# Optimization experiments

Measured on AMD Instinct MI355X. Metric: run time of the kernel, lower is better.

The kernel has to match this reference:

```python
import jax, jax.numpy as jnp
import numpy as np

DIM = 2048
STATE = 16
BATCH = 2
SEQ = 2048
LN_EPS = 1e-5


def setup_inputs() -> dict:
    key = jax.random.key(0)
    ks = jax.random.split(key, 12)
    d, n = DIM, STATE
    inp = {
        "x": jax.random.normal(ks[0], (BATCH, SEQ, d), dtype=jnp.float32),
        "ln_gamma": jnp.ones((d,), dtype=jnp.float32),
        "ln_beta": jnp.zeros((d,), dtype=jnp.float32),
        # proj_in: Linear(d, 2d) (spectral-normed; weights treated as effective)
        "W_in": jax.random.normal(ks[1], (2 * d, d), dtype=jnp.float32) / np.sqrt(d),
        "b_in": jnp.zeros((2 * d,), dtype=jnp.float32),
        "state_A": jax.random.normal(ks[2], (n, d), dtype=jnp.float32) * 0.01,
        "W_B": jax.random.normal(ks[3], (n, d), dtype=jnp.float32) / np.sqrt(d),
        "b_B": jnp.zeros((n,), dtype=jnp.float32),
        "W_C": jax.random.normal(ks[4], (n, d), dtype=jnp.float32) / np.sqrt(d),
        "b_C": jnp.zeros((n,), dtype=jnp.float32),
        "W_dt": jax.random.normal(ks[5], (d, d), dtype=jnp.float32) / np.sqrt(d),
        "b_dt": jnp.zeros((d,), dtype=jnp.float32),
        "W_out": jax.random.normal(ks[6], (d, d), dtype=jnp.float32) / np.sqrt(d),
        "b_out": jnp.zeros((d,), dtype=jnp.float32),
    }
    return inp


def reference(x, ln_gamma, ln_beta, W_in, b_in, state_A, W_B, b_B, W_C, b_C,
              W_dt, b_dt, W_out, b_out):
    residual = x
    # LayerNorm over last dim
    mu = jnp.mean(x, axis=-1, keepdims=True)
    var = jnp.mean(jnp.square(x - mu), axis=-1, keepdims=True)
    xn = (x - mu) * jax.lax.rsqrt(var + LN_EPS) * ln_gamma + ln_beta
    # input projection and gate split
    xz = jnp.einsum('bsd,ed->bse', xn, W_in) + b_in          # (B,S,2D)
    x_ssm, z = jnp.split(xz, 2, axis=-1)                      # (B,S,D) each
    # dt = clamp(softplus(proj_dt(x_ssm)), max=1.0)
    dt = jnp.minimum(jax.nn.softplus(jnp.einsum('bsd,ed->bse', x_ssm, W_dt) + b_dt), 1.0)
    Bm = jnp.einsum('bsd,nd->bsn', x_ssm, W_B) + b_B          # (B,S,N)
    Cm = jnp.einsum('bsd,nd->bsn', x_ssm, W_C) + b_C          # (B,S,N)
    # A_bar[b,s,n,d] = exp(state_A[n,d] * dt[b,s,d])
    A_bar = jnp.exp(state_A[None, None, :, :] * dt[:, :, None, :])  # (B,S,N,D)
    # y[b,s,d] = sum_n C[b,s,n]*B[b,s,n]*A_bar[b,s,n,d] * x_ssm[b,s,d]
    y = jnp.einsum('bsn,bsnd->bsd', Cm * Bm, A_bar) * x_ssm
    gated = y * jax.nn.silu(z)
    out = jnp.einsum('bsd,ed->bse', gated, W_out) + b_out
    return out + residual
```

## Files before the change

### kernel.cpp

```cpp
#include <hip/hip_runtime.h>

typedef unsigned short u16;
typedef float f32x4 __attribute__((ext_vector_type(4)));
typedef __bf16 bf16x8 __attribute__((ext_vector_type(8)));

__device__ __forceinline__ u16 f2bf(float f) {
    unsigned u = __float_as_uint(f);
    u += 0x7FFFu + ((u >> 16) & 1u);
    return (u16)(u >> 16);
}
__device__ __forceinline__ float b2f(u16 h) {
    return __uint_as_float(((unsigned)h) << 16);
}

__device__ __forceinline__ void async16(const u16* g, u16* l) {
    __builtin_amdgcn_global_load_lds(
        (__attribute__((address_space(1))) void*)(u16*)g,
        (__attribute__((address_space(3))) void*)l,
        16, 0, 0);
}

#define T_TOK 4096
#define DIM   2048

__global__ __launch_bounds__(256) void castln_kernel(const float* __restrict__ W_in,
                                                     u16* __restrict__ wb_in,
                                                     const float* __restrict__ x,
                                                     const float* __restrict__ g,
                                                     const float* __restrict__ b,
                                                     u16* __restrict__ o) {
    __shared__ float s1[4], s2[4];
    int blk = blockIdx.x, tid = threadIdx.x;
    if (blk < 8192) {
        int i = blk * 256 + tid;
        float4 f = ((const float4*)W_in)[i];
        ushort4 u;
        u.x = f2bf(f.x); u.y = f2bf(f.y); u.z = f2bf(f.z); u.w = f2bf(f.w);
        ((ushort4*)wb_in)[i] = u;
        return;
    }
    int t = blk - 8192;
    int wave = tid >> 6, lane = tid & 63;
    size_t base = (size_t)t * DIM;
    int d0 = tid * 8;
    float4 v0 = *(const float4*)(x + base + d0);
    float4 v1 = *(const float4*)(x + base + d0 + 4);
    float v[8] = {v0.x, v0.y, v0.z, v0.w, v1.x, v1.y, v1.z, v1.w};
    float s = 0.f;
#pragma unroll
    for (int j = 0; j < 8; ++j) s += v[j];
#pragma unroll
    for (int o2 = 32; o2; o2 >>= 1) s += __shfl_xor(s, o2);
    if (lane == 0) s1[wave] = s;
    __syncthreads();
    float mu = (s1[0] + s1[1] + s1[2] + s1[3]) * (1.f / DIM);
    float q = 0.f;
#pragma unroll
    for (int j = 0; j < 8; ++j) { float dd = v[j] - mu; q += dd * dd; }
#pragma unroll
    for (int o2 = 32; o2; o2 >>= 1) q += __shfl_xor(q, o2);
    if (lane == 0) s2[wave] = q;
    __syncthreads();
    float var = (s2[0] + s2[1] + s2[2] + s2[3]) * (1.f / DIM);
    float rs = rsqrtf(var + 1e-5f);
    float4 g0 = *(const float4*)(g + d0), g1 = *(const float4*)(g + d0 + 4);
    float4 b0 = *(const float4*)(b + d0), b1 = *(const float4*)(b + d0 + 4);
    float gv[8] = {g0.x, g0.y, g0.z, g0.w, g1.x, g1.y, g1.z, g1.w};
    float bv[8] = {b0.x, b0.y, b0.z, b0.w, b1.x, b1.y, b1.z, b1.w};
    ushort4 r0, r1;
    u16* rp0 = (u16*)&r0; u16* rp1 = (u16*)&r1;
#pragma unroll
    for (int j = 0; j < 4; ++j) {
        rp0[j] = f2bf((v[j] - mu) * rs * gv[j] + bv[j]);
        rp1[j] = f2bf((v[j + 4] - mu) * rs * gv[j + 4] + bv[j + 4]);
    }
    *(ushort4*)(o + base + d0) = r0;
    *(ushort4*)(o + base + d0 + 4) = r1;
}

__global__ __launch_bounds__(256) void cast4_kernel(const float* __restrict__ s0, u16* __restrict__ d0, int n0,
                                                    const float* __restrict__ s1, u16* __restrict__ d1, int n1,
                                                    const float* __restrict__ s2, u16* __restrict__ d2, int n2,
                                                    const float* __restrict__ s3, u16* __restrict__ d3, int n3) {
    int j = blockIdx.x * 256 + threadIdx.x;
    const float* s; u16* d;
    if (j < n0) { s = s0; d = d0; }
    else {
        j -= n0;
        if (j < n1) { s = s1; d = d1; }
        else {
            j -= n1;
            if (j < n2) { s = s2; d = d2; }
            else { j -= n2; if (j >= n3) return; s = s3; d = d3; }
        }
    }
    float4 f = ((const float4*)s)[j];
    ushort4 u;
    u.x = f2bf(f.x); u.y = f2bf(f.y); u.z = f2bf(f.z); u.w = f2bf(f.w);
    ((ushort4*)d)[j] = u;
}

#define GBM 256
#define GBN 256
#define GBK 64

#define WAITV4 asm volatile("s_waitcnt vmcnt(4)" ::: "memory")
#define SBAR() do { __builtin_amdgcn_sched_barrier(0); __builtin_amdgcn_s_barrier(); } while (0)

__global__ __launch_bounds__(512) void gemm_wide(const u16* __restrict__ A,
                                                 const u16* __restrict__ W,
                                                 const float* __restrict__ bias,
                                                 u16* __restrict__ Xs,
                                                 u16* __restrict__ Z, int K) {
    __shared__ __align__(16) u16 lA[2][GBM * GBK];
    __shared__ __align__(16) u16 lB[2][GBN * GBK];
    const int tid = threadIdx.x;
    const int wv = tid >> 6, lane = tid & 63;
    const int quad = lane >> 4, l16 = lane & 15;
    const int wr = wv >> 2, wc = wv & 3;
    const int tM = blockIdx.x * GBM, tN = blockIdx.y * GBN;

    const int srow = tid >> 3;
    const int swz = ((tid & 7) ^ (srow & 7)) * 8;
    const u16* gA = A + (size_t)(tM + srow) * 2048 + swz;
    const u16* gW = W + (size_t)(tN + srow) * 2048 + swz;

#define STAGE_A(BI, KC) do {                                                  \
    _Pragma("unroll") for (int r_ = 0; r_ < 4; ++r_)                          \
      async16(gA + (size_t)r_ * 64 * 2048 + (KC),                             \
              &lA[BI][(r_ * 64 + wv * 8) * GBK]);                             \
  } while (0)
#define STAGE_B(BI, KC) do {                                                  \
    _Pragma("unroll") for (int r_ = 0; r_ < 4; ++r_)                          \
      async16(gW + (size_t)r_ * 64 * 2048 + (KC),                             \
              &lB[BI][(r_ * 64 + wv * 8) * GBK]);                             \
  } while (0)

    int aoff[2][4][2], boff[2][2][2];
#pragma unroll
    for (int qm = 0; qm < 2; ++qm)
#pragma unroll
        for (int mi = 0; mi < 4; ++mi)
#pragma unroll
            for (int h = 0; h < 2; ++h) {
                int row = wr * 128 + (qm * 4 + mi) * 16 + l16;
                aoff[qm][mi][h] = row * GBK + (((h * 4 + quad) ^ (l16 & 7)) * 8);
            }
#pragma unroll
    for (int qn = 0; qn < 2; ++qn)
#pragma unroll
        for (int ni = 0; ni < 2; ++ni)
#pragma unroll
            for (int h = 0; h < 2; ++h) {
                int row = wc * 64 + (qn * 2 + ni) * 16 + l16;
                boff[qn][ni][h] = row * GBK + (((h * 4 + quad) ^ (l16 & 7)) * 8);
            }

    f32x4 acc[8][4] = {};
    bf16x8 af[4][2];

#define PHASE(BI, QM, QN, LOADA, STAGE_STMT, WAIT_STMT) do {                  \
    if (LOADA) {                                                              \
      _Pragma("unroll") for (int mi_ = 0; mi_ < 4; ++mi_)                     \
        _Pragma("unroll") for (int h_ = 0; h_ < 2; ++h_)                      \
          af[mi_][h_] = *(const bf16x8*)&lA[BI][aoff[QM][mi_][h_]];           \
    }                                                                         \
    bf16x8 bfr_[2][2];                                                        \
    _Pragma("unroll") for (int ni_ = 0; ni_ < 2; ++ni_)                       \
      _Pragma("unroll") for (int h_ = 0; h_ < 2; ++h_)                        \
        bfr_[ni_][h_] = *(const bf16x8*)&lB[BI][boff[QN][ni_][h_]];           \
    STAGE_STMT;                                                               \
    SBAR();                                                                   \
    __builtin_amdgcn_s_setprio(1);                                            \
    _Pragma("unroll") for (int mi_ = 0; mi_ < 4; ++mi_)                       \
      _Pragma("unroll") for (int ni_ = 0; ni_ < 2; ++ni_)                     \
        _Pragma("unroll") for (int h_ = 0; h_ < 2; ++h_)                      \
          acc[QM * 4 + mi_][QN * 2 + ni_] =                                   \
              __builtin_amdgcn_mfma_f32_16x16x32_bf16(                        \
                  af[mi_][h_], bfr_[ni_][h_],                                 \
                  acc[QM * 4 + mi_][QN * 2 + ni_], 0, 0, 0);                  \
    __builtin_amdgcn_s_setprio(0);                                            \
    WAIT_STMT;                                                                \
    SBAR();                                                                   \
  } while (0)

    STAGE_A(0, 0);
    STAGE_B(0, 0);
    STAGE_A(1, 64);
    WAITV4;
    SBAR();

    const int NIT = K >> 7;
    for (int it = 0; it < NIT; ++it) {
        const int k1 = it * 128 + 64;
        int kn = it * 128 + 128;
        if (kn > K - 64) kn = K - 64;
        int kn1 = it * 128 + 192;
        if (kn1 > K - 64) kn1 = K - 64;

        PHASE(0, 0, 0, 1, STAGE_B(1, k1), (void)0);
        PHASE(0, 0, 1, 0, (void)0,        (void)0);
        PHASE(0, 1, 0, 1, (void)0,        (void)0);
        PHASE(0, 1, 1, 0, STAGE_A(0, kn), WAITV4);
        PHASE(1, 0, 0, 1, STAGE_B(0, kn), (void)0);
        PHASE(1, 0, 1, 0, (void)0,        (void)0);
        PHASE(1, 1, 0, 1, (void)0,        (void)0);
        PHASE(1, 1, 1, 0, STAGE_A(1, kn1), WAITV4);
    }

    asm volatile("s_waitcnt vmcnt(0)" ::: "memory");

    const bool isb_z = (tN >= 2048);
    u16* dst = isb_z ? Z : Xs;
#pragma unroll
    for (int mi = 0; mi < 8; ++mi) {
#pragma unroll
        for (int ni = 0; ni < 4; ++ni) {
            int col = tN + wc * 64 + ni * 16 + l16;
            float bv = bias[col];
            int ocol = isb_z ? (col - 2048) : col;
#pragma unroll
            for (int r = 0; r < 4; ++r) {
                int row = tM + wr * 128 + mi * 16 + quad * 4 + r;
                dst[(size_t)row * 2048 + ocol] = f2bf(acc[mi][ni][r] + bv);
            }
        }
    }
#undef PHASE
#undef STAGE_A
#undef STAGE_B
}

#define NBM 128
#define NBN 64
#define NBK 64

template <int EPI>
__global__ __launch_bounds__(256) void gemm_nw(const u16* __restrict__ A, int lda,
                                               const u16* __restrict__ W, int ldw,
                                               const float* __restrict__ bias,
                                               const float* __restrict__ resid,
                                               void* __restrict__ C, int ldc, int K,
                                               u16* __restrict__ dots) {
    __shared__ __align__(16) u16 lAB[(NBM + NBN) * NBK];
    const int tid = threadIdx.x;
    const int wave = tid >> 6, lane = tid & 63;
    const int quad = lane >> 4, l16 = lane & 15;
    const int tM = blockIdx.x * NBM;
    const int tN = blockIdx.y * NBN;
    const int wr = wave >> 1, wc = wave & 1;

    const int rowin = tid >> 3;
    const int r3 = rowin & 7;
    const int col8 = ((tid & 7) ^ r3) * 8;
    const u16* gptr[6];
    u16* ldst[6];
#pragma unroll
    for (int i = 0; i < 6; ++i) {
        int trow = i * 32 + rowin;
        const u16* src = (i < 4) ? (A + (size_t)(tM + trow) * lda)
                                 : (W + (size_t)(tN + (trow - NBM)) * ldw);
        gptr[i] = src + col8;
        ldst[i] = &lAB[(i * 32 + wave * 8) * NBK];
    }

    int a_off[2][4], b_off[2][2];
#pragma unroll
    for (int h = 0; h < 2; ++h) {
#pragma unroll
        for (int mi = 0; mi < 4; ++mi)
            a_off[h][mi] = (wr * 64 + mi * 16 + l16) * NBK +
                           (((h * 4 + quad) ^ (l16 & 7)) * 8);
#pragma unroll
        for (int ni = 0; ni < 2; ++ni)
            b_off[h][ni] = (NBM + wc * 32 + ni * 16 + l16) * NBK +
                           (((h * 4 + quad) ^ (l16 & 7)) * 8);
    }

    f32x4 acc[4][2] = {};

    for (int kt = 0; kt < K; kt += NBK) {
#pragma unroll
        for (int i = 0; i < 6; ++i) async16(gptr[i] + kt, ldst[i]);
        __syncthreads();
        bf16x8 af[2][4], bfr[2][2];
#pragma unroll
        for (int h = 0; h < 2; ++h) {
#pragma unroll
            for (int mi = 0; mi < 4; ++mi) af[h][mi] = *(const bf16x8*)&lAB[a_off[h][mi]];
#pragma unroll
            for (int ni = 0; ni < 2; ++ni) bfr[h][ni] = *(const bf16x8*)&lAB[b_off[h][ni]];
        }
#pragma unroll
        for (int h = 0; h < 2; ++h)
#pragma unroll
            for (int mi = 0; mi < 4; ++mi)
#pragma unroll
                for (int ni = 0; ni < 2; ++ni)
                    acc[mi][ni] = __builtin_amdgcn_mfma_f32_16x16x32_bf16(
                        af[h][mi], bfr[h][ni], acc[mi][ni], 0, 0, 0);
        __syncthreads();
    }

#pragma unroll
    for (int mi = 0; mi < 4; ++mi) {
#pragma unroll
        for (int ni = 0; ni < 2; ++ni) {
            int col = tN + wc * 32 + ni * 16 + l16;
            float bv = (EPI == 1 && col >= 2048) ? 0.f : bias[col];
#pragma unroll
            for (int r = 0; r < 4; ++r) {
                int row = tM + wr * 64 + mi * 16 + quad * 4 + r;
                float v = acc[mi][ni][r] + bv;
                if constexpr (EPI == 1) {
                    if (col < 2048) {
                        float sp = (v > 20.f) ? v : log1pf(__expf(v));
                        ((u16*)C)[(size_t)row * ldc + col] = f2bf(fminf(sp, 1.0f));
                    } else if (col < 2080) {
                        dots[(size_t)row * 32 + (col - 2048)] = f2bf(v);
                    }
                } else {
                    size_t idx = (size_t)row * ldc + col;
                    ((float*)C)[idx] = v + resid[idx];
                }
            }
        }
    }
}

__global__ __launch_bounds__(256) void ssm_gate_kernel(const u16* __restrict__ dtb,
                                                       const u16* __restrict__ xsb,
                                                       const u16* __restrict__ zb,
                                                       const float* __restrict__ A,
                                                       const u16* __restrict__ dots,
                                                       const float* __restrict__ bB,
                                                       const float* __restrict__ bC,
                                                       u16* __restrict__ gated) {
    __shared__ float Pl[16];
    int t = blockIdx.x, tid = threadIdx.x;
    if (tid < 16) {
        float Bv = b2f(dots[(size_t)t * 32 + tid]) + bB[tid];
        float Cv = b2f(dots[(size_t)t * 32 + 16 + tid]) + bC[tid];
        Pl[tid] = Bv * Cv;
    }
    __syncthreads();
    size_t dbase = (size_t)t * DIM;
    int d0 = tid * 8;
    ushort4 dth[2], xsh[2], zh[2];
    dth[0] = *(const ushort4*)(dtb + dbase + d0);
    dth[1] = *(const ushort4*)(dtb + dbase + d0 + 4);
    xsh[0] = *(const ushort4*)(xsb + dbase + d0);
    xsh[1] = *(const ushort4*)(xsb + dbase + d0 + 4);
    zh[0]  = *(const ushort4*)(zb + dbase + d0);
    zh[1]  = *(const ushort4*)(zb + dbase + d0 + 4);
    float dtv[8], xsv[8], zv[8];
#pragma unroll
    for (int h = 0; h < 2; ++h) {
        const u16* dp = (const u16*)&dth[h];
        const u16* xp = (const u16*)&xsh[h];
        const u16* zp = (const u16*)&zh[h];
#pragma unroll
        for (int j = 0; j < 4; ++j) {
            dtv[h * 4 + j] = b2f(dp[j]);
            xsv[h * 4 + j] = b2f(xp[j]);
            zv[h * 4 + j]  = b2f(zp[j]);
        }
    }
    float s[8] = {};
#pragma unroll
    for (int n = 0; n < 16; ++n) {
        float4 a0 = *(const float4*)(A + n * DIM + d0);
        float4 a1 = *(const float4*)(A + n * DIM + d0 + 4);
        float pn = Pl[n];
        float av[8] = {a0.x, a0.y, a0.z, a0.w, a1.x, a1.y, a1.z, a1.w};
#pragma unroll
        for (int j = 0; j < 8; ++j) s[j] += pn * __expf(av[j] * dtv[j]);
    }
    ushort4 r0, r1;
    u16* rp0 = (u16*)&r0; u16* rp1 = (u16*)&r1;
#pragma unroll
    for (int j = 0; j < 8; ++j) {
        float y = s[j] * xsv[j];
        float sz = zv[j] * (1.0f / (1.0f + __expf(-zv[j])));
        u16 hv = f2bf(y * sz);
        if (j < 4) rp0[j] = hv; else rp1[j - 4] = hv;
    }
    *(ushort4*)(gated + dbase + d0) = r0;
    *(ushort4*)(gated + dbase + d0 + 4) = r1;
}

extern "C" void kernel_launch(void* const* d_in, const int* in_sizes, int n_in,
                              void* d_out, int out_size, void* d_ws, size_t ws_size,
                              hipStream_t stream) {
    const float* x      = (const float*)d_in[0];
    const float* ln_g   = (const float*)d_in[1];
    const float* ln_b   = (const float*)d_in[2];
    const float* W_in   = (const float*)d_in[3];
    const float* b_in   = (const float*)d_in[4];
    const float* stateA = (const float*)d_in[5];
    const float* W_B    = (const float*)d_in[6];
    const float* b_B    = (const float*)d_in[7];
    const float* W_C    = (const float*)d_in[8];
    const float* b_C    = (const float*)d_in[9];
    const float* W_dt   = (const float*)d_in[10];
    const float* b_dt   = (const float*)d_in[11];
    const float* W_out  = (const float*)d_in[12];
    const float* b_out  = (const float*)d_in[13];

    char* ws = (char*)d_ws;
    u16*   wb_in  = (u16*)(ws);
    u16*   wb_out = (u16*)(ws);
    u16*   xnb    = (u16*)(ws + 16777216);
    u16*   wb_dt  = (u16*)(ws + 16777216);
    u16*   gated  = (u16*)(ws + 16777216);
    u16*   xsb    = (u16*)(ws + 33554432);
    u16*   zb     = (u16*)(ws + 50331648);
    u16*   dtb    = (u16*)(ws + 67108864);
    u16*   dotsb  = (u16*)(ws + 83886080);

    castln_kernel<<<12288, 256, 0, stream>>>(W_in, wb_in, x, ln_g, ln_b, xnb);
    gemm_wide<<<dim3(16, 16), 512, 0, stream>>>(xnb, wb_in, b_in, xsb, zb, 2048);
    cast4_kernel<<<8256, 256, 0, stream>>>(
        W_dt, wb_dt, 1048576,
        W_B,  wb_dt + (size_t)2048 * 2048, 8192,
        W_C,  wb_dt + (size_t)2064 * 2048, 8192,
        W_out, wb_out, 1048576);
    gemm_nw<1><<<dim3(32, 33), 256, 0, stream>>>(xsb, 2048, wb_dt, 2048, b_dt,
                                                 nullptr, dtb, 2048, 2048, dotsb);
    ssm_gate_kernel<<<T_TOK, 256, 0, stream>>>(dtb, xsb, zb, stateA, dotsb,
                                               b_B, b_C, gated);
    gemm_nw<2><<<dim3(32, 32), 256, 0, stream>>>(gated, 2048, wb_out, 2048, b_out,
                                                 x, (float*)d_out, 2048, 2048, nullptr);
}
```

Before: 385.6 us.

## Use 256x256 pipelined GEMM for dt and output projections with snake fragment reuse

Replaces the smaller 128x64 GEMM kernel used for the dt/B/C and output projections with the 256x256 double-buffered, 8-wave GEMM, templated on three epilogues (split store, softplus/dots, bias plus residual). The phase order is changed to a snake pattern so B fragments are reused across consecutive phases, which skips some LDS reads. Explicit lgkmcnt waits replace some scheduling barriers. The aim is higher data reuse and MFMA efficiency per block. The trade-off is that the grids shrink to 144 and 128 blocks, which leaves many CUs idle on a 256-CU part, and the dt GEMM now reads padded weight rows past 2080.

```diff
diff --git a/kernel.cpp b/kernel.cpp
--- a/kernel.cpp
+++ b/kernel.cpp
@@ -104,14 +104,13 @@
 #define GBN 256
 #define GBK 64
 
-#define WAITV4 asm volatile("s_waitcnt vmcnt(4)" ::: "memory")
-#define SBAR() do { __builtin_amdgcn_sched_barrier(0); __builtin_amdgcn_s_barrier(); } while (0)
-
-__global__ __launch_bounds__(512) void gemm_wide(const u16* __restrict__ A,
-                                                 const u16* __restrict__ W,
-                                                 const float* __restrict__ bias,
-                                                 u16* __restrict__ Xs,
-                                                 u16* __restrict__ Z, int K) {
+template <int EPI>
+__global__ __launch_bounds__(512) void gemm256(const u16* __restrict__ A,
+                                               const u16* __restrict__ W,
+                                               const float* __restrict__ bias,
+                                               const float* __restrict__ resid,
+                                               void* __restrict__ C0,
+                                               void* __restrict__ C1, int K) {
     __shared__ __align__(16) u16 lA[2][GBM * GBK];
     __shared__ __align__(16) u16 lB[2][GBN * GBK];
     const int tid = threadIdx.x;
@@ -157,38 +156,43 @@
             }
 
     f32x4 acc[8][4] = {};
-    bf16x8 af[4][2];
-
-#define PHASE(BI, QM, QN, LOADA, STAGE_STMT, WAIT_STMT) do {                  \
+    bf16x8 af[4][2], bfr[2][2];
+
+#define PHASE(BI, QM, QN, LOADA, LOADB, HINT12, STAGE_STMT, DOWAIT) do {      \
     if (LOADA) {                                                              \
       _Pragma("unroll") for (int mi_ = 0; mi_ < 4; ++mi_)                     \
         _Pragma("unroll") for (int h_ = 0; h_ < 2; ++h_)                      \
           af[mi_][h_] = *(const bf16x8*)&lA[BI][aoff[QM][mi_][h_]];           \
     }                                                                         \
-    bf16x8 bfr_[2][2];                                                        \
-    _Pragma("unroll") for (int ni_ = 0; ni_ < 2; ++ni_)                       \
-      _Pragma("unroll") for (int h_ = 0; h_ < 2; ++h_)                        \
-        bfr_[ni_][h_] = *(const bf16x8*)&lB[BI][boff[QN][ni_][h_]];           \
+    if (LOADB) {                                                              \
+      _Pragma("unroll") for (int ni_ = 0; ni_ < 2; ++ni_)                     \
+        _Pragma("unroll") for (int h_ = 0; h_ < 2; ++h_)                      \
+          bfr[ni_][h_] = *(const bf16x8*)&lB[BI][boff[QN][ni_][h_]];          \
+    }                                                                         \
     STAGE_STMT;                                                               \
-    SBAR();                                                                   \
+    if (HINT12) asm volatile("s_waitcnt lgkmcnt(8)");                         \
+    __builtin_amdgcn_s_barrier();                                             \
+    asm volatile("s_waitcnt lgkmcnt(0)");                                     \
     __builtin_amdgcn_s_setprio(1);                                            \
     _Pragma("unroll") for (int mi_ = 0; mi_ < 4; ++mi_)                       \
       _Pragma("unroll") for (int ni_ = 0; ni_ < 2; ++ni_)                     \
         _Pragma("unroll") for (int h_ = 0; h_ < 2; ++h_)                      \
           acc[QM * 4 + mi_][QN * 2 + ni_] =                                   \
               __builtin_amdgcn_mfma_f32_16x16x32_bf16(                        \
-                  af[mi_][h_], bfr_[ni_][h_],                                 \
+                  af[mi_][h_], bfr[ni_][h_],                                  \
                   acc[QM * 4 + mi_][QN * 2 + ni_], 0, 0, 0);                  \
     __builtin_amdgcn_s_setprio(0);                                            \
-    WAIT_STMT;                                                                \
-    SBAR();                                                                   \
+    if (DOWAIT) asm volatile("s_waitcnt vmcnt(4)" ::: "memory");              \
+    __builtin_amdgcn_s_barrier();                                             \
+    if (DOWAIT) __builtin_amdgcn_sched_barrier(0);                            \
   } while (0)
 
     STAGE_A(0, 0);
     STAGE_B(0, 0);
     STAGE_A(1, 64);
-    WAITV4;
-    SBAR();
+    asm volatile("s_waitcnt vmcnt(4)" ::: "memory");
+    __builtin_amdgcn_s_barrier();
+    __builtin_amdgcn_sched_barrier(0);
 
     const int NIT = K >> 7;
     for (int it = 0; it < NIT; ++it) {
@@ -198,134 +202,65 @@
         int kn1 = it * 128 + 192;
         if (kn1 > K - 64) kn1 = K - 64;
 
-        PHASE(0, 0, 0, 1, STAGE_B(1, k1), (void)0);
-        PHASE(0, 0, 1, 0, (void)0,        (void)0);
-        PHASE(0, 1, 0, 1, (void)0,        (void)0);
-        PHASE(0, 1, 1, 0, STAGE_A(0, kn), WAITV4);
-        PHASE(1, 0, 0, 1, STAGE_B(0, kn), (void)0);
-        PHASE(1, 0, 1, 0, (void)0,        (void)0);
-        PHASE(1, 1, 0, 1, (void)0,        (void)0);
-        PHASE(1, 1, 1, 0, STAGE_A(1, kn1), WAITV4);
+        PHASE(0, 0, 0, 1, 1, 1, STAGE_B(1, k1),  0);
+        PHASE(0, 0, 1, 0, 1, 0, (void)0,         0);
+        PHASE(0, 1, 1, 1, 0, 0, (void)0,         0);
+        PHASE(0, 1, 0, 0, 1, 0, STAGE_A(0, kn),  1);
+        PHASE(1, 0, 0, 1, 1, 1, STAGE_B(0, kn),  0);
+        PHASE(1, 0, 1, 0, 1, 0, (void)0,         0);
+        PHASE(1, 1, 1, 1, 0, 0, (void)0,         0);
+        PHASE(1, 1, 0, 0, 1, 0, STAGE_A(1, kn1), 1);
     }
 
     asm volatile("s_waitcnt vmcnt(0)" ::: "memory");
 
-    const bool isb_z = (tN >= 2048);
-    u16* dst = isb_z ? Z : Xs;
 #pragma unroll
     for (int mi = 0; mi < 8; ++mi) {
 #pragma unroll
         for (int ni = 0; ni < 4; ++ni) {
             int col = tN + wc * 64 + ni * 16 + l16;
-            float bv = bias[col];
-            int ocol = isb_z ? (col - 2048) : col;
-#pragma unroll
-            for (int r = 0; r < 4; ++r) {
-                int row = tM + wr * 128 + mi * 16 + quad * 4 + r;
-                dst[(size_t)row * 2048 + ocol] = f2bf(acc[mi][ni][r] + bv);
+            if constexpr (EPI == 0) {
+                const bool isb_z = (tN >= 2048);
+                u16* dst = isb_z ? (u16*)C1 : (u16*)C0;
+                float bv = bias[col];
+                int ocol = isb_z ? (col - 2048) : col;
+#pragma unroll
+                for (int r = 0; r < 4; ++r) {
+                    int row = tM + wr * 128 + mi * 16 + quad * 4 + r;
+                    dst[(size_t)row * 2048 + ocol] = f2bf(acc[mi][ni][r] + bv);
+                }
+            } else if constexpr (EPI == 1) {
+                if (col < 2048) {
+                    float bv = bias[col];
+#pragma unroll
+                    for (int r = 0; r < 4; ++r) {
+                        int row = tM + wr * 128 + mi * 16 + quad * 4 + r;
+                        float v = acc[mi][ni][r] + bv;
+                        float sp = (v > 20.f) ? v : log1pf(__expf(v));
+                        ((u16*)C0)[(size_t)row * 2048 + col] = f2bf(fminf(sp, 1.0f));
+                    }
+                } else if (col < 2080) {
+#pragma unroll
+                    for (int r = 0; r < 4; ++r) {
+                        int row = tM + wr * 128 + mi * 16 + quad * 4 + r;
+                        ((u16*)C1)[(size_t)row * 32 + (col - 2048)] =
+                            f2bf(acc[mi][ni][r]);
+                    }
+                }
+            } else {
+                float bv = bias[col];
+#pragma unroll
+                for (int r = 0; r < 4; ++r) {
+                    int row = tM + wr * 128 + mi * 16 + quad * 4 + r;
+                    size_t idx = (size_t)row * 2048 + col;
+                    ((float*)C0)[idx] = acc[mi][ni][r] + bv + resid[idx];
+                }
             }
         }
     }
 #undef PHASE
 #undef STAGE_A
 #undef STAGE_B
-}
-
-#define NBM 128
-#define NBN 64
-#define NBK 64
-
-template <int EPI>
-__global__ __launch_bounds__(256) void gemm_nw(const u16* __restrict__ A, int lda,
-                                               const u16* __restrict__ W, int ldw,
-                                               const float* __restrict__ bias,
-                                               const float* __restrict__ resid,
-                                               void* __restrict__ C, int ldc, int K,
-                                               u16* __restrict__ dots) {
-    __shared__ __align__(16) u16 lAB[(NBM + NBN) * NBK];
-    const int tid = threadIdx.x;
-    const int wave = tid >> 6, lane = tid & 63;
-    const int quad = lane >> 4, l16 = lane & 15;
-    const int tM = blockIdx.x * NBM;
-    const int tN = blockIdx.y * NBN;
-    const int wr = wave >> 1, wc = wave & 1;
-
-    const int rowin = tid >> 3;
-    const int r3 = rowin & 7;
-    const int col8 = ((tid & 7) ^ r3) * 8;
-    const u16* gptr[6];
-    u16* ldst[6];
-#pragma unroll
-    for (int i = 0; i < 6; ++i) {
-        int trow = i * 32 + rowin;
-        const u16* src = (i < 4) ? (A + (size_t)(tM + trow) * lda)
-                                 : (W + (size_t)(tN + (trow - NBM)) * ldw);
-        gptr[i] = src + col8;
-        ldst[i] = &lAB[(i * 32 + wave * 8) * NBK];
-    }
-
-    int a_off[2][4], b_off[2][2];
-#pragma unroll
-    for (int h = 0; h < 2; ++h) {
-#pragma unroll
-        for (int mi = 0; mi < 4; ++mi)
-            a_off[h][mi] = (wr * 64 + mi * 16 + l16) * NBK +
-                           (((h * 4 + quad) ^ (l16 & 7)) * 8);
-#pragma unroll
-        for (int ni = 0; ni < 2; ++ni)
-            b_off[h][ni] = (NBM + wc * 32 + ni * 16 + l16) * NBK +
-                           (((h * 4 + quad) ^ (l16 & 7)) * 8);
-    }
-
-    f32x4 acc[4][2] = {};
-
-    for (int kt = 0; kt < K; kt += NBK) {
-#pragma unroll
-        for (int i = 0; i < 6; ++i) async16(gptr[i] + kt, ldst[i]);
-        __syncthreads();
-        bf16x8 af[2][4], bfr[2][2];
-#pragma unroll
-        for (int h = 0; h < 2; ++h) {
-#pragma unroll
-            for (int mi = 0; mi < 4; ++mi) af[h][mi] = *(const bf16x8*)&lAB[a_off[h][mi]];
-#pragma unroll
-            for (int ni = 0; ni < 2; ++ni) bfr[h][ni] = *(const bf16x8*)&lAB[b_off[h][ni]];
-        }
-#pragma unroll
-        for (int h = 0; h < 2; ++h)
-#pragma unroll
-            for (int mi = 0; mi < 4; ++mi)
-#pragma unroll
-                for (int ni = 0; ni < 2; ++ni)
-                    acc[mi][ni] = __builtin_amdgcn_mfma_f32_16x16x32_bf16(
-                        af[h][mi], bfr[h][ni], acc[mi][ni], 0, 0, 0);
-        __syncthreads();
-    }
-
-#pragma unroll
-    for (int mi = 0; mi < 4; ++mi) {
-#pragma unroll
-        for (int ni = 0; ni < 2; ++ni) {
-            int col = tN + wc * 32 + ni * 16 + l16;
-            float bv = (EPI == 1 && col >= 2048) ? 0.f : bias[col];
-#pragma unroll
-            for (int r = 0; r < 4; ++r) {
-                int row = tM + wr * 64 + mi * 16 + quad * 4 + r;
-                float v = acc[mi][ni][r] + bv;
-                if constexpr (EPI == 1) {
-                    if (col < 2048) {
-                        float sp = (v > 20.f) ? v : log1pf(__expf(v));
-                        ((u16*)C)[(size_t)row * ldc + col] = f2bf(fminf(sp, 1.0f));
-                    } else if (col < 2080) {
-                        dots[(size_t)row * 32 + (col - 2048)] = f2bf(v);
-                    }
-                } else {
-                    size_t idx = (size_t)row * ldc + col;
-                    ((float*)C)[idx] = v + resid[idx];
-                }
-            }
-        }
-    }
 }
 
 __global__ __launch_bounds__(256) void ssm_gate_kernel(const u16* __restrict__ dtb,
@@ -419,16 +354,17 @@
     u16*   dotsb  = (u16*)(ws + 83886080);
 
     castln_kernel<<<12288, 256, 0, stream>>>(W_in, wb_in, x, ln_g, ln_b, xnb);
-    gemm_wide<<<dim3(16, 16), 512, 0, stream>>>(xnb, wb_in, b_in, xsb, zb, 2048);
+    gemm256<0><<<dim3(16, 16), 512, 0, stream>>>(xnb, wb_in, b_in, nullptr,
+                                                 xsb, zb, 2048);
     cast4_kernel<<<8256, 256, 0, stream>>>(
         W_dt, wb_dt, 1048576,
         W_B,  wb_dt + (size_t)2048 * 2048, 8192,
         W_C,  wb_dt + (size_t)2064 * 2048, 8192,
         W_out, wb_out, 1048576);
-    gemm_nw<1><<<dim3(32, 33), 256, 0, stream>>>(xsb, 2048, wb_dt, 2048, b_dt,
-                                                 nullptr, dtb, 2048, 2048, dotsb);
+    gemm256<1><<<dim3(16, 9), 512, 0, stream>>>(xsb, wb_dt, b_dt, nullptr,
+                                                dtb, dotsb, 2048);
     ssm_gate_kernel<<<T_TOK, 256, 0, stream>>>(dtb, xsb, zb, stateA, dotsb,
                                                b_B, b_C, gated);
-    gemm_nw<2><<<dim3(32, 32), 256, 0, stream>>>(gated, 2048, wb_out, 2048, b_out,
-                                                 x, (float*)d_out, 2048, 2048, nullptr);
-}
+    gemm256<2><<<dim3(16, 8), 512, 0, stream>>>(gated, wb_out, b_out, x,
+                                                (float*)d_out, nullptr, 2048);
+}
```

Measured after the change: 449.0 us. 16.4% more time.
